# Performance work log

Hardware: AMD Instinct MI355X
Metric: run time of the kernel (lower is better)

Reference implementation:

```python
import jax, jax.numpy as jnp
import numpy as np

B_, L_, D_, N_ = 4, 4096, 1024, 32


def setup_inputs() -> dict:
    key = jax.random.key(0)
    ks = jax.random.split(key, 8)
    def n(k, shape, s=0.02):
        return jax.random.normal(k, shape, jnp.float32) * s
    return {
        "x": jax.random.normal(ks[0], (B_, L_, D_), jnp.float32),
        "in_w": n(ks[1], (2 * D_, D_)),
        "in_b": jnp.zeros((2 * D_,), jnp.float32),
        "conv_w": n(ks[2], (D_, 1, 4), 0.1),
        "conv_b": jnp.zeros((D_,), jnp.float32),
        "A_log": -2.0 + 0.1 * jax.random.normal(ks[3], (D_, N_), jnp.float32),
        "B_w": n(ks[4], (N_, D_)),
        "B_b": jnp.zeros((N_,), jnp.float32),
        "C_w": n(ks[5], (N_, D_)),
        "C_b": jnp.zeros((N_,), jnp.float32),
        "out_w": n(ks[6], (D_, D_)),
        "out_b": jnp.zeros((D_,), jnp.float32),
        "ln_w": jnp.ones((D_,), jnp.float32),
        "ln_b": jnp.zeros((D_,), jnp.float32),
    }


def reference(x, in_w, in_b, conv_w, conv_b, A_log, B_w, B_b, C_w, C_b, out_w, out_b, ln_w, ln_b):
    Bsz, L, D = x.shape
    residual = x
    # in_proj and chunk
    xz = x @ in_w.T + in_b                       # (B, L, 2D)
    xa, z = xz[..., :D], xz[..., D:]
    # depthwise conv1d, kernel=4, padding=2 -> length L+1 (matches torch)
    xc = jax.lax.conv_general_dilated(
        xa.transpose(0, 2, 1), conv_w, (1,), [(2, 2)],
        feature_group_count=D, dimension_numbers=("NCH", "OIH", "NCH"))
    xc = xc + conv_b[None, :, None]
    xc = jax.nn.silu(xc.transpose(0, 2, 1))      # (B, L+1, D)
    A = -jnp.exp(jnp.clip(A_log, -5.0, 2.0))     # (D, N)
    Bm = xc @ B_w.T + B_b                        # (B, L+1, N)
    Cm = xc @ C_w.T + C_b                        # (B, L+1, N)
    # only first L steps are used by the loop
    xs = (xc[:, :L].transpose(1, 0, 2),          # (L, B, D)
          Bm[:, :L].transpose(1, 0, 2),          # (L, B, N)
          Cm[:, :L].transpose(1, 0, 2))          # (L, B, N)
    s0 = jnp.zeros((Bsz, D, A.shape[1]), x.dtype)

    def step(s, t):
        x_t, b_t, c_t = t
        s = jnp.clip(s * A + b_t[:, None, :] * x_t[:, :, None], -10.0, 10.0)
        y = jnp.sum(c_t[:, None, :] * s, axis=-1)  # (B, D)
        return s, y

    _, ys = jax.lax.scan(step, s0, xs)           # ys: (L, B, D)
    y = ys.transpose(1, 0, 2) * jax.nn.silu(z)   # (B, L, D)
    out = y @ out_w.T + out_b
    h = out + residual
    mu = jnp.mean(h, axis=-1, keepdims=True)
    var = jnp.var(h, axis=-1, keepdims=True)
    return (h - mu) / jnp.sqrt(var + 1e-5) * ln_w + ln_b
```

## Files before the change

kernel.cpp:

```cpp
#include <hip/hip_runtime.h>
#include <hip/hip_bf16.h>

#define B_ 4
#define L_ 4096
#define D_ 1024
#define N_ 32
#define MTOT (B_*L_)
#define TCH 32
#define WARM 6
#define STEPS (TCH + WARM)
#define SROWS 48

typedef __bf16 bf16;
typedef __attribute__((ext_vector_type(8))) __bf16 bf16x8;
typedef __attribute__((ext_vector_type(4))) __bf16 bf16x4;
typedef __attribute__((ext_vector_type(4))) float f32x4;
typedef __attribute__((ext_vector_type(2))) float f32x2;

__device__ __forceinline__ void gload_lds16(const void* gsrc, void* ldst) {
  __builtin_amdgcn_global_load_lds(
      (__attribute__((address_space(1))) void*)(unsigned long long)gsrc,
      (__attribute__((address_space(3))) void*)ldst, 16, 0, 0);
}

#define BARR  do { __builtin_amdgcn_s_barrier(); \
                   __builtin_amdgcn_sched_barrier(0); } while (0)
#define LGKM0 do { asm volatile("s_waitcnt lgkmcnt(0)" ::: "memory"); \
                   __builtin_amdgcn_sched_barrier(0); } while (0)

__global__ __launch_bounds__(256) void cvt_w_kernel(
    const float* __restrict__ in_w, const float* __restrict__ out_w,
    const float* __restrict__ B_w, const float* __restrict__ C_w,
    const float* __restrict__ A_log, const float* __restrict__ B_b,
    const float* __restrict__ C_b, const float* __restrict__ x,
    bf16* __restrict__ in_wb, bf16* __restrict__ out_wb, bf16* __restrict__ bcw,
    float* __restrict__ Aexp, float* __restrict__ bias_bc,
    bf16* __restrict__ xb) {
  const int stride = gridDim.x * 256;
  const int i0 = blockIdx.x * 256 + threadIdx.x;
  for (int j = i0; j < (B_ * L_ * D_) / 4; j += stride) {
    const float4 v = ((const float4*)x)[j];
    bf16x4 o = {(bf16)v.x, (bf16)v.y, (bf16)v.z, (bf16)v.w};
    ((bf16x4*)xb)[j] = o;
  }
  for (int j = i0; j < 2 * D_ * D_; j += stride) in_wb[j] = (bf16)in_w[j];
  for (int j = i0; j < D_ * D_; j += stride) out_wb[j] = (bf16)out_w[j];
  for (int j = i0; j < N_ * D_; j += stride) {
    bcw[j] = (bf16)B_w[j];
    bcw[N_ * D_ + j] = (bf16)C_w[j];
  }
  for (int j = i0; j < D_ * N_; j += stride)
    Aexp[j] = -expf(fminf(fmaxf(A_log[j], -5.f), 2.f));
  if (i0 < N_) { bias_bc[i0] = B_b[i0]; bias_bc[N_ + i0] = C_b[i0]; }
}

template <bool OUT_BF16>
__global__ __launch_bounds__(256) void gemm8_kernel(
    const bf16* __restrict__ Ag, const bf16* __restrict__ Wg,
    const float* __restrict__ bias, void* __restrict__ Cg,
    int Ncols, int K, int nbm, int nbn) {
  constexpr int BK = 64;
  __shared__ bf16 As[2][128][64];
  __shared__ bf16 Bs[2][128][64];
  const int tid = threadIdx.x;
  const int lane = tid & 63;
  const int wid = tid >> 6;
  const int wm = wid >> 1, wn = wid & 1;
  const int l15 = lane & 15, lh = lane >> 4, r7 = l15 & 7;

  const int sx = nbm >> 3;
  const int xcd = blockIdx.x & 7;
  const int pos = blockIdx.x >> 3;
  const int bx = xcd * sx + pos / nbn;
  const int by = pos % nbn;
  const int row0 = bx * 128, col0 = by * 128;
  const int nt = K / BK;

  const bf16* aSrc[4]; const bf16* bSrc[4]; int dstOff[4];
#pragma unroll
  for (int j = 0; j < 4; ++j) {
    const int c = tid + j * 256;
    const int row = c >> 3, lcol = c & 7;
    const int gcol = lcol ^ (row & 7);
    aSrc[j] = Ag + (size_t)(row0 + row) * K + gcol * 8;
    bSrc[j] = Wg + (size_t)(col0 + row) * K + gcol * 8;
    dstOff[j] = c * 8;
  }

  f32x4 acc[4][4] = {};

#pragma unroll
  for (int j = 0; j < 4; ++j) gload_lds16(aSrc[j], &As[0][0][0] + dstOff[j]);
#pragma unroll
  for (int j = 0; j < 4; ++j) gload_lds16(bSrc[j], &Bs[0][0][0] + dstOff[j]);
#pragma unroll
  for (int j = 0; j < 4; ++j) gload_lds16(aSrc[j] + BK, &As[1][0][0] + dstOff[j]);
#pragma unroll
  for (int j = 0; j < 4; ++j) gload_lds16(bSrc[j] + BK, &Bs[1][0][0] + dstOff[j]);
  asm volatile("s_waitcnt vmcnt(8)" ::: "memory");
  __builtin_amdgcn_sched_barrier(0);
  BARR;

  for (int t = 0; t < nt; ++t) {
    const int p = t & 1;
    const bf16* Ab = &As[p][0][0];
    const bf16* Bb = &Bs[p][0][0];
    bf16x8 af[4][2], bfr[4][2];
#pragma unroll
    for (int mi = 0; mi < 4; ++mi)
#pragma unroll
      for (int kk = 0; kk < 2; ++kk)
        af[mi][kk] = *(const bf16x8*)(Ab + (wm * 64 + mi * 16 + l15) * 64 +
                                      (((kk * 4 + lh) ^ r7) * 8));
#pragma unroll
    for (int ni = 0; ni < 4; ++ni)
#pragma unroll
      for (int kk = 0; kk < 2; ++kk)
        bfr[ni][kk] = *(const bf16x8*)(Bb + (wn * 64 + ni * 16 + l15) * 64 +
                                       (((kk * 4 + lh) ^ r7) * 8));
    LGKM0;
    BARR;
    if (t + 2 < nt) {
      const int k2 = (t + 2) * BK;
#pragma unroll
      for (int j = 0; j < 4; ++j) gload_lds16(aSrc[j] + k2, &As[p][0][0] + dstOff[j]);
#pragma unroll
      for (int j = 0; j < 4; ++j) gload_lds16(bSrc[j] + k2, &Bs[p][0][0] + dstOff[j]);
    }
    __builtin_amdgcn_s_setprio(1);
#pragma unroll
    for (int kk = 0; kk < 2; ++kk)
#pragma unroll
      for (int mi = 0; mi < 4; ++mi)
#pragma unroll
        for (int ni = 0; ni < 4; ++ni)
          acc[mi][ni] = __builtin_amdgcn_mfma_f32_16x16x32_bf16(
              af[mi][kk], bfr[ni][kk], acc[mi][ni], 0, 0, 0);
    __builtin_amdgcn_s_setprio(0);
    if (t + 2 < nt) asm volatile("s_waitcnt vmcnt(8)" ::: "memory");
    else            asm volatile("s_waitcnt vmcnt(0)" ::: "memory");
    __builtin_amdgcn_sched_barrier(0);
    BARR;
  }

#pragma unroll
  for (int mi = 0; mi < 4; ++mi) {
#pragma unroll
    for (int ni = 0; ni < 4; ++ni) {
      const int c = col0 + wn * 64 + ni * 16 + l15;
      const float bv = bias[c];
#pragma unroll
      for (int j = 0; j < 4; ++j) {
        const int r = row0 + wm * 64 + mi * 16 + lh * 4 + j;
        const float v = acc[mi][ni][j] + bv;
        if constexpr (OUT_BF16) ((bf16*)Cg)[(size_t)r * Ncols + c] = (bf16)v;
        else                    ((float*)Cg)[(size_t)r * Ncols + c] = v;
      }
    }
  }
}

__global__ __launch_bounds__(256) void gemmbc_kernel(
    const bf16* __restrict__ Ag, const bf16* __restrict__ Wg,
    const float* __restrict__ bias, float* __restrict__ Cg, int K) {
  constexpr int BK = 64;
  __shared__ bf16 As[2][64][64];
  __shared__ bf16 Bs[2][64][64];
  const int tid = threadIdx.x;
  const int lane = tid & 63;
  const int wid = tid >> 6;
  const int wm = wid >> 1, wn = wid & 1;
  const int l15 = lane & 15, lh = lane >> 4;
  const int row0 = blockIdx.x * 64;
  const int nt = K / BK;

  const bf16* aSrc[2]; const bf16* bSrc[2]; int dstOff[2];
#pragma unroll
  for (int j = 0; j < 2; ++j) {
    const int c = tid + j * 256;
    const int row = c >> 3, lcol = c & 7;
    const int gcol = lcol ^ (row & 7);
    aSrc[j] = Ag + (size_t)(row0 + row) * K + gcol * 8;
    bSrc[j] = Wg + (size_t)row * K + gcol * 8;
    dstOff[j] = c * 8;
  }

  f32x4 acc[2][2] = {};

#pragma unroll
  for (int j = 0; j < 2; ++j) gload_lds16(aSrc[j], &As[0][0][0] + dstOff[j]);
#pragma unroll
  for (int j = 0; j < 2; ++j) gload_lds16(bSrc[j], &Bs[0][0][0] + dstOff[j]);
#pragma unroll
  for (int j = 0; j < 2; ++j) gload_lds16(aSrc[j] + BK, &As[1][0][0] + dstOff[j]);
#pragma unroll
  for (int j = 0; j < 2; ++j) gload_lds16(bSrc[j] + BK, &Bs[1][0][0] + dstOff[j]);
  asm volatile("s_waitcnt vmcnt(4)" ::: "memory");
  __builtin_amdgcn_sched_barrier(0);
  BARR;

  for (int t = 0; t < nt; ++t) {
    const int p = t & 1;
    const bf16* Ab = &As[p][0][0];
    const bf16* Bb = &Bs[p][0][0];
    bf16x8 af[2][2], bfr[2][2];
#pragma unroll
    for (int mi = 0; mi < 2; ++mi)
#pragma unroll
      for (int kk = 0; kk < 2; ++kk) {
        const int r = wm * 32 + mi * 16 + l15;
        af[mi][kk] = *(const bf16x8*)(Ab + r * 64 + (((kk * 4 + lh) ^ (r & 7)) * 8));
      }
#pragma unroll
    for (int ni = 0; ni < 2; ++ni)
#pragma unroll
      for (int kk = 0; kk < 2; ++kk) {
        const int r = wn * 32 + ni * 16 + l15;
        bfr[ni][kk] = *(const bf16x8*)(Bb + r * 64 + (((kk * 4 + lh) ^ (r & 7)) * 8));
      }
    LGKM0;
    BARR;
    if (t + 2 < nt) {
      const int k2 = (t + 2) * BK;
#pragma unroll
      for (int j = 0; j < 2; ++j) gload_lds16(aSrc[j] + k2, &As[p][0][0] + dstOff[j]);
#pragma unroll
      for (int j = 0; j < 2; ++j) gload_lds16(bSrc[j] + k2, &Bs[p][0][0] + dstOff[j]);
    }
    __builtin_amdgcn_s_setprio(1);
#pragma unroll
    for (int kk = 0; kk < 2; ++kk)
#pragma unroll
      for (int mi = 0; mi < 2; ++mi)
#pragma unroll
        for (int ni = 0; ni < 2; ++ni)
          acc[mi][ni] = __builtin_amdgcn_mfma_f32_16x16x32_bf16(
              af[mi][kk], bfr[ni][kk], acc[mi][ni], 0, 0, 0);
    __builtin_amdgcn_s_setprio(0);
    if (t + 2 < nt) asm volatile("s_waitcnt vmcnt(4)" ::: "memory");
    else            asm volatile("s_waitcnt vmcnt(0)" ::: "memory");
    __builtin_amdgcn_sched_barrier(0);
    BARR;
  }

#pragma unroll
  for (int mi = 0; mi < 2; ++mi) {
#pragma unroll
    for (int ni = 0; ni < 2; ++ni) {
      const int c = wn * 32 + ni * 16 + l15;
      const float bv = bias[c];
#pragma unroll
      for (int j = 0; j < 4; ++j) {
        const int r = row0 + wm * 32 + mi * 16 + lh * 4 + j;
        Cg[(size_t)r * 64 + c] = acc[mi][ni][j] + bv;
      }
    }
  }
}

__global__ __launch_bounds__(512, 1) void gemm256_kernel(
    const bf16* __restrict__ Ag, const bf16* __restrict__ Wg,
    const float* __restrict__ bias, bf16* __restrict__ Cg,
    int Ncols, int K, int nbm, int nbn) {
  __shared__ bf16 lds[8][128][64];
  const int tid = threadIdx.x;
  const int lane = tid & 63;
  const int wid = tid >> 6;
  const int wm = wid >> 2;
  const int wn = wid & 3;
  const int l15 = lane & 15, lh = lane >> 4;

  const int sx = nbm >> 3;
  const int xcd = blockIdx.x & 7;
  const int pos = blockIdx.x >> 3;
  const int bx = xcd * sx + pos / nbn;
  const int by = pos % nbn;
  const int row0 = bx * 256, col0 = by * 256;
  const int nt = K / 64;

  const bf16* aS0; const bf16* aS1; const bf16* bS0; const bf16* bS1;
  int dO0, dO1;
  {
    const int c0 = tid, c1 = tid + 512;
    const int r0 = c0 >> 3, r1 = c1 >> 3;
    const int g0 = (c0 & 7) ^ (r0 & 7), g1 = (c1 & 7) ^ (r1 & 7);
    aS0 = Ag + (size_t)(row0 + r0) * K + g0 * 8;
    aS1 = Ag + (size_t)(row0 + r1) * K + g1 * 8;
    bS0 = Wg + (size_t)(col0 + r0) * K + g0 * 8;
    bS1 = Wg + (size_t)(col0 + r1) * K + g1 * 8;
    dO0 = c0 * 8; dO1 = c1 * 8;
  }

#define STAGE_A(T, HALF) do {                                               \
    const size_t off_ = (size_t)(HALF) * 128 * K + (size_t)(T) * 64;        \
    bf16* dst_ = &lds[((T) & 1) * 4 + (HALF)][0][0];                        \
    gload_lds16(aS0 + off_, dst_ + dO0);                                    \
    gload_lds16(aS1 + off_, dst_ + dO1); } while (0)
#define STAGE_B(T, HALF) do {                                               \
    const size_t off_ = (size_t)(HALF) * 128 * K + (size_t)(T) * 64;        \
    bf16* dst_ = &lds[((T) & 1) * 4 + 2 + (HALF)][0][0];                    \
    gload_lds16(bS0 + off_, dst_ + dO0);                                    \
    gload_lds16(bS1 + off_, dst_ + dO1); } while (0)

  f32x4 acc[8][4] = {};

  STAGE_A(0, 0); STAGE_A(0, 1); STAGE_B(0, 0); STAGE_B(0, 1);
  STAGE_B(1, 0); STAGE_B(1, 1);
  asm volatile("s_waitcnt vmcnt(4)" ::: "memory");
  __builtin_amdgcn_sched_barrier(0);
  BARR;

  for (int T = 0; T < nt; ++T) {
    const int p = T & 1;
    const bf16* Aseg = &lds[p * 4 + wm][0][0];
    const bf16* Bseg = &lds[p * 4 + 2 + (wn >> 1)][0][0];
    const int brow0 = (wn & 1) * 64;
    bf16x8 af[4][2], bfv[4][2];
    const bool s1 = (T + 1 < nt), s2 = (T + 2 < nt);

    if (s1) STAGE_A(T + 1, 0);
#pragma unroll
    for (int mi = 0; mi < 4; ++mi) {
      const int r = mi * 16 + l15, sw = r & 7;
      af[mi][0] = *(const bf16x8*)(Aseg + r * 64 + ((lh ^ sw)) * 8);
      af[mi][1] = *(const bf16x8*)(Aseg + r * 64 + (((4 + lh) ^ sw)) * 8);
    }
#pragma unroll
    for (int ni = 0; ni < 2; ++ni) {
      const int r = brow0 + ni * 16 + l15, sw = r & 7;
      bfv[ni][0] = *(const bf16x8*)(Bseg + r * 64 + ((lh ^ sw)) * 8);
      bfv[ni][1] = *(const bf16x8*)(Bseg + r * 64 + (((4 + lh) ^ sw)) * 8);
    }
    BARR; LGKM0;
    __builtin_amdgcn_s_setprio(1);
#pragma unroll
    for (int kk = 0; kk < 2; ++kk)
#pragma unroll
      for (int mi = 0; mi < 4; ++mi)
#pragma unroll
        for (int ni = 0; ni < 2; ++ni)
          acc[mi][ni] = __builtin_amdgcn_mfma_f32_16x16x32_bf16(
              af[mi][kk], bfv[ni][kk], acc[mi][ni], 0, 0, 0);
    __builtin_amdgcn_s_setprio(0);
    BARR;

    if (s1) STAGE_A(T + 1, 1);
#pragma unroll
    for (int ni = 2; ni < 4; ++ni) {
      const int r = brow0 + ni * 16 + l15, sw = r & 7;
      bfv[ni][0] = *(const bf16x8*)(Bseg + r * 64 + ((lh ^ sw)) * 8);
      bfv[ni][1] = *(const bf16x8*)(Bseg + r * 64 + (((4 + lh) ^ sw)) * 8);
    }
    BARR; LGKM0;
    __builtin_amdgcn_s_setprio(1);
#pragma unroll
    for (int kk = 0; kk < 2; ++kk)
#pragma unroll
      for (int mi = 0; mi < 4; ++mi)
#pragma unroll
        for (int ni = 2; ni < 4; ++ni)
          acc[mi][ni] = __builtin_amdgcn_mfma_f32_16x16x32_bf16(
              af[mi][kk], bfv[ni][kk], acc[mi][ni], 0, 0, 0);
    __builtin_amdgcn_s_setprio(0);
    BARR;

    if (s2) STAGE_B(T + 2, 0);
#pragma unroll
    for (int mi = 0; mi < 4; ++mi) {
      const int r = (mi + 4) * 16 + l15, sw = r & 7;
      af[mi][0] = *(const bf16x8*)(Aseg + r * 64 + ((lh ^ sw)) * 8);
      af[mi][1] = *(const bf16x8*)(Aseg + r * 64 + (((4 + lh) ^ sw)) * 8);
    }
    BARR; LGKM0;
    __builtin_amdgcn_s_setprio(1);
#pragma unroll
    for (int kk = 0; kk < 2; ++kk)
#pragma unroll
      for (int mi = 0; mi < 4; ++mi)
#pragma unroll
        for (int ni = 0; ni < 2; ++ni)
          acc[mi + 4][ni] = __builtin_amdgcn_mfma_f32_16x16x32_bf16(
              af[mi][kk], bfv[ni][kk], acc[mi + 4][ni], 0, 0, 0);
    __builtin_amdgcn_s_setprio(0);
    BARR;

    if (s2) STAGE_B(T + 2, 1);
    BARR;
    __builtin_amdgcn_s_setprio(1);
#pragma unroll
    for (int kk = 0; kk < 2; ++kk)
#pragma unroll
      for (int mi = 0; mi < 4; ++mi)
#pragma unroll
        for (int ni = 2; ni < 4; ++ni)
          acc[mi + 4][ni] = __builtin_amdgcn_mfma_f32_16x16x32_bf16(
              af[mi][kk], bfv[ni][kk], acc[mi + 4][ni], 0, 0, 0);
    __builtin_amdgcn_s_setprio(0);
    if (s2) asm volatile("s_waitcnt vmcnt(4)" ::: "memory");
    else    asm volatile("s_waitcnt vmcnt(0)" ::: "memory");
    __builtin_amdgcn_sched_barrier(0);
    BARR;
  }
#undef STAGE_A
#undef STAGE_B

#pragma unroll
  for (int mi = 0; mi < 8; ++mi) {
#pragma unroll
    for (int ni = 0; ni < 4; ++ni) {
      const int c = col0 + wn * 64 + ni * 16 + l15;
      const float bv = bias[c];
#pragma unroll
      for (int j = 0; j < 4; ++j) {
        const int r = row0 + wm * 128 + mi * 16 + lh * 4 + j;
        Cg[(size_t)r * Ncols + c] = (bf16)(acc[mi][ni][j] + bv);
      }
    }
  }
}

__global__ __launch_bounds__(256) void conv_silu_kernel(
    const bf16* __restrict__ xz, const float* __restrict__ conv_w,
    const float* __restrict__ conv_b, bf16* __restrict__ xc) {
  const int idx = blockIdx.x * 256 + threadIdx.x;
  const int d8 = idx & (D_ / 8 - 1);
  const int bt = idx >> 7;
  const int t = bt & (L_ - 1);
  const int b = bt >> 12;
  const int d = d8 * 8;

  float accv[8];
  float4 w4[8];
#pragma unroll
  for (int j = 0; j < 8; ++j) {
    accv[j] = conv_b[d + j];
    w4[j] = *(const float4*)(conv_w + (size_t)(d + j) * 4);
  }
#pragma unroll
  for (int k = 0; k < 4; ++k) {
    const int tt = t + k - 2;
    if (tt < 0 || tt >= L_) continue;
    const bf16x8 xv = *(const bf16x8*)(xz + (size_t)(b * L_ + tt) * (2 * D_) + d);
#pragma unroll
    for (int j = 0; j < 8; ++j) {
      const float wk = (k == 0) ? w4[j].x : (k == 1) ? w4[j].y : (k == 2) ? w4[j].z : w4[j].w;
      accv[j] += (float)xv[j] * wk;
    }
  }
  bf16x8 o;
#pragma unroll
  for (int j = 0; j < 8; ++j) {
    const float v = accv[j];
    o[j] = (bf16)(v / (1.f + __expf(-v)));
  }
  *(bf16x8*)(xc + (size_t)(b * L_ + t) * D_ + d) = o;
}

#define SCAN_STEP(PB, PC, XT)                                             \
  {                                                                       \
    const f32x2 xt2 = {XT, XT};                                           \
    yac = (f32x2){0.f, 0.f};                                              \
    _Pragma("unroll")                                                     \
    for (int q = 0; q < 8; ++q) {                                         \
      f32x2 v = __builtin_elementwise_fma(s[q], Ar[q], PB[q] * xt2);      \
      s[q] = v;                                                           \
      yac = __builtin_elementwise_fma(PC[q], v, yac);                     \
    }                                                                     \
  }

__device__ __forceinline__ void load8v(f32x2* dst, const float* p) {
#pragma unroll
  for (int q = 0; q < 4; ++q) {
    const f32x4 v = ((const f32x4*)p)[q];
    dst[2 * q]     = (f32x2){v.x, v.y};
    dst[2 * q + 1] = (f32x2){v.z, v.w};
  }
}

__global__ __launch_bounds__(256)
__attribute__((amdgpu_waves_per_eu(4)))
void scan_kernel(
    const bf16* __restrict__ xc, const float* __restrict__ BC,
    const bf16* __restrict__ xz, const float* __restrict__ Aexp,
    bf16* __restrict__ y) {
  const int dg = blockIdx.x, chunk = blockIdx.y, b = blockIdx.z;
  const int tid = threadIdx.x;
  const int wid = tid >> 6;
  const int nh = tid & 1;
  const int dl = tid >> 1;
  const int d = dg * 128 + dl;
  const int t0 = chunk * TCH;
  const int warm = (t0 >= WARM) ? WARM : 0;
  const int tstart = t0 - warm;

  __shared__ float bcs[SROWS][64];
  __shared__ bf16 xcs[SROWS][128];
  __shared__ bf16 zs[TCH][128];

#pragma unroll
  for (int i = 0; i < 3; ++i)
    gload_lds16(BC + ((size_t)b * L_ + tstart) * 64 + (size_t)(tid + i * 256) * 4,
                (float*)&bcs[0][0] + (size_t)(wid * 64 + i * 256) * 4);
#pragma unroll
  for (int i = 0; i < 3; ++i) {
    const int c = tid + i * 256;
    gload_lds16(xc + ((size_t)b * L_ + tstart + (c >> 4)) * D_ + dg * 128 + (c & 15) * 8,
                (bf16*)&xcs[0][0] + (size_t)(wid * 64 + i * 256) * 8);
  }
#pragma unroll
  for (int i = 0; i < 2; ++i) {
    const int c = tid + i * 256;
    gload_lds16(xz + ((size_t)b * L_ + t0 + (c >> 4)) * (2 * D_) + D_ + dg * 128 + (c & 15) * 8,
                (bf16*)&zs[0][0] + (size_t)(wid * 64 + i * 256) * 8);
  }

  f32x2 Ar[8], s[8];
  {
    const f32x2* ap = (const f32x2*)(Aexp + (size_t)d * N_ + nh * 16);
#pragma unroll
    for (int q = 0; q < 8; ++q) { Ar[q] = ap[q]; s[q] = (f32x2){0.f, 0.f}; }
  }

  bf16* yp = y + (size_t)b * L_ * D_ + d;
  f32x2 yac;

  __syncthreads();

  for (int i = 0; i < warm; ++i) {
    const float xt = (float)xcs[i][dl];
    const f32x2 xt2 = {xt, xt};
    const f32x2* rb = (const f32x2*)&bcs[i][nh * 16];
#pragma unroll
    for (int q = 0; q < 8; ++q)
      s[q] = __builtin_elementwise_fma(s[q], Ar[q], rb[q] * xt2);
  }

  f32x2 pbA[8], pcA[8], pbB[8], pcB[8];
  float pxA, pzA, pxB, pzB;
  load8v(pbA, &bcs[warm][nh * 16]);
  load8v(pcA, &bcs[warm][32 + nh * 16]);
  pxA = (float)xcs[warm][dl];
  pzA = (float)zs[0][dl];

  for (int j = 0; j < TCH; j += 2) {
    load8v(pbB, &bcs[warm + j + 1][nh * 16]);
    load8v(pcB, &bcs[warm + j + 1][32 + nh * 16]);
    pxB = (float)xcs[warm + j + 1][dl];
    pzB = (float)zs[j + 1][dl];
    SCAN_STEP(pbA, pcA, pxA);
    {
      float yacc = yac.x + yac.y;
      yacc += __shfl_xor(yacc, 1);
      if (nh == 0) {
        const float sz = pzA / (1.f + __expf(-pzA));
        yp[(size_t)(t0 + j) * D_] = (bf16)(yacc * sz);
      }
    }
    load8v(pbA, &bcs[warm + j + 2][nh * 16]);
    load8v(pcA, &bcs[warm + j + 2][32 + nh * 16]);
    pxA = (float)xcs[warm + j + 2][dl];
    pzA = (float)zs[(j + 2 < TCH) ? (j + 2) : 0][dl];
    SCAN_STEP(pbB, pcB, pxB);
    {
      float yacc = yac.x + yac.y;
      yacc += __shfl_xor(yacc, 1);
      if (nh == 0) {
        const float sz = pzB / (1.f + __expf(-pzB));
        yp[(size_t)(t0 + j + 1) * D_] = (bf16)(yacc * sz);
      }
    }
  }
}

__global__ __launch_bounds__(256) void ln2_kernel(const bf16* __restrict__ g,
                                                  const float* __restrict__ x,
                                                  const float* __restrict__ ln_w,
                                                  const float* __restrict__ ln_b,
                                                  float* __restrict__ out) {
  const int row = blockIdx.x;
  const int tid = threadIdx.x;
  const bf16x4 gv = ((const bf16x4*)(g + (size_t)row * D_))[tid];
  const float4 xv = ((const float4*)(x + (size_t)row * D_))[tid];
  float4 v;
  v.x = (float)gv[0] + xv.x;
  v.y = (float)gv[1] + xv.y;
  v.z = (float)gv[2] + xv.z;
  v.w = (float)gv[3] + xv.w;
  float sum = v.x + v.y + v.z + v.w;
  float sq = v.x * v.x + v.y * v.y + v.z * v.z + v.w * v.w;
#pragma unroll
  for (int off = 32; off >= 1; off >>= 1) {
    sum += __shfl_xor(sum, off);
    sq += __shfl_xor(sq, off);
  }
  __shared__ float red[8];
  const int wid = tid >> 6;
  if ((tid & 63) == 0) { red[wid] = sum; red[4 + wid] = sq; }
  __syncthreads();
  sum = red[0] + red[1] + red[2] + red[3];
  sq = red[4] + red[5] + red[6] + red[7];
  const float mu = sum * (1.f / D_);
  const float var = sq * (1.f / D_) - mu * mu;
  const float inv = rsqrtf(var + 1e-5f);
  const float4 w4 = ((const float4*)ln_w)[tid];
  const float4 b4 = ((const float4*)ln_b)[tid];
  float4 o;
  o.x = (v.x - mu) * inv * w4.x + b4.x;
  o.y = (v.y - mu) * inv * w4.y + b4.y;
  o.z = (v.z - mu) * inv * w4.z + b4.z;
  o.w = (v.w - mu) * inv * w4.w + b4.w;
  ((float4*)(out + (size_t)row * D_))[tid] = o;
}

extern "C" void kernel_launch(void* const* d_in, const int* in_sizes, int n_in,
                              void* d_out, int out_size, void* d_ws, size_t ws_size,
                              hipStream_t stream) {
  (void)in_sizes; (void)n_in; (void)out_size; (void)ws_size;
  const float* x      = (const float*)d_in[0];
  const float* in_w   = (const float*)d_in[1];
  const float* in_b   = (const float*)d_in[2];
  const float* conv_w = (const float*)d_in[3];
  const float* conv_b = (const float*)d_in[4];
  const float* A_log  = (const float*)d_in[5];
  const float* B_w    = (const float*)d_in[6];
  const float* B_b    = (const float*)d_in[7];
  const float* C_w    = (const float*)d_in[8];
  const float* C_b    = (const float*)d_in[9];
  const float* out_w  = (const float*)d_in[10];
  const float* out_b  = (const float*)d_in[11];
  const float* ln_w   = (const float*)d_in[12];
  const float* ln_b   = (const float*)d_in[13];
  float* out = (float*)d_out;

  char* ws = (char*)d_ws;
  bf16* xb_y    = (bf16*)(ws + 0);
  bf16* xz      = (bf16*)(ws + 33554432);
  bf16* xc_g    = (bf16*)(ws + 100663296);
  float* BC     = (float*)(ws + 134217728);
  bf16* in_wb   = (bf16*)(ws + 138412032);
  bf16* out_wb  = (bf16*)(ws + 142606336);
  bf16* bcw     = (bf16*)(ws + 144703488);
  float* Aexp   = (float*)(ws + 144834560);
  float* bias_bc= (float*)(ws + 144965632);

  cvt_w_kernel<<<2048, 256, 0, stream>>>(in_w, out_w, B_w, C_w, A_log, B_b, C_b,
                                         x, in_wb, out_wb, bcw, Aexp, bias_bc, xb_y);
  gemm8_kernel<true>
      <<<128 * 16, 256, 0, stream>>>(xb_y, in_wb, in_b, xz, 2 * D_, D_, 128, 16);
  conv_silu_kernel<<<(B_ * L_ * D_ / 8) / 256, 256, 0, stream>>>(xz, conv_w, conv_b, xc_g);
  gemmbc_kernel<<<MTOT / 64, 256, 0, stream>>>(xc_g, bcw, bias_bc, BC, D_);
  scan_kernel<<<dim3(D_ / 128, L_ / TCH, B_), 256, 0, stream>>>(xc_g, BC, xz, Aexp, xb_y);
  gemm256_kernel<<<64 * 4, 512, 0, stream>>>(xb_y, out_wb, out_b, xc_g,
                                             D_, D_, 64, 4);
  ln2_kernel<<<MTOT, 256, 0, stream>>>(xc_g, x, ln_w, ln_b, out);
}
```

Baseline: 294.4 us.

## Write scan output into xz's x-half, keep bf16 x for residual in LayerNorm

The scan now writes y into the unused first half of the xz buffer, with a row stride of 2D, and the output GEMM reads A through a new lda parameter. The original bf16 copy of x is therefore kept intact, and the final LayerNorm reads that bf16 residual instead of the fp32 input, halving the residual read traffic. The scan kernel's waves_per_eu hint is loosened to a 2–4 range. The risks are lower residual precision from using bf16 instead of fp32, and a strided A access pattern in the GEMM.

```diff
diff --git a/kernel.cpp b/kernel.cpp
--- a/kernel.cpp
+++ b/kernel.cpp
@@ -261,7 +261,7 @@
 __global__ __launch_bounds__(512, 1) void gemm256_kernel(
     const bf16* __restrict__ Ag, const bf16* __restrict__ Wg,
     const float* __restrict__ bias, bf16* __restrict__ Cg,
-    int Ncols, int K, int nbm, int nbn) {
+    int Ncols, int K, int lda, int nbm, int nbn) {
   __shared__ bf16 lds[8][128][64];
   const int tid = threadIdx.x;
   const int lane = tid & 63;
@@ -284,15 +284,15 @@
     const int c0 = tid, c1 = tid + 512;
     const int r0 = c0 >> 3, r1 = c1 >> 3;
     const int g0 = (c0 & 7) ^ (r0 & 7), g1 = (c1 & 7) ^ (r1 & 7);
-    aS0 = Ag + (size_t)(row0 + r0) * K + g0 * 8;
-    aS1 = Ag + (size_t)(row0 + r1) * K + g1 * 8;
+    aS0 = Ag + (size_t)(row0 + r0) * lda + g0 * 8;
+    aS1 = Ag + (size_t)(row0 + r1) * lda + g1 * 8;
     bS0 = Wg + (size_t)(col0 + r0) * K + g0 * 8;
     bS1 = Wg + (size_t)(col0 + r1) * K + g1 * 8;
     dO0 = c0 * 8; dO1 = c1 * 8;
   }
 
 #define STAGE_A(T, HALF) do {                                               \
-    const size_t off_ = (size_t)(HALF) * 128 * K + (size_t)(T) * 64;        \
+    const size_t off_ = (size_t)(HALF) * 128 * lda + (size_t)(T) * 64;      \
     bf16* dst_ = &lds[((T) & 1) * 4 + (HALF)][0][0];                        \
     gload_lds16(aS0 + off_, dst_ + dO0);                                    \
     gload_lds16(aS1 + off_, dst_ + dO1); } while (0)
@@ -478,11 +478,11 @@
 }
 
 __global__ __launch_bounds__(256)
-__attribute__((amdgpu_waves_per_eu(4)))
+__attribute__((amdgpu_waves_per_eu(2, 4)))
 void scan_kernel(
     const bf16* __restrict__ xc, const float* __restrict__ BC,
     const bf16* __restrict__ xz, const float* __restrict__ Aexp,
-    bf16* __restrict__ y) {
+    bf16* __restrict__ yz) {
   const int dg = blockIdx.x, chunk = blockIdx.y, b = blockIdx.z;
   const int tid = threadIdx.x;
   const int wid = tid >> 6;
@@ -521,7 +521,7 @@
     for (int q = 0; q < 8; ++q) { Ar[q] = ap[q]; s[q] = (f32x2){0.f, 0.f}; }
   }
 
-  bf16* yp = y + (size_t)b * L_ * D_ + d;
+  bf16* yp = yz + (size_t)b * L_ * (2 * D_) + d;
   f32x2 yac;
 
   __syncthreads();
@@ -553,7 +553,7 @@
       yacc += __shfl_xor(yacc, 1);
       if (nh == 0) {
         const float sz = pzA / (1.f + __expf(-pzA));
-        yp[(size_t)(t0 + j) * D_] = (bf16)(yacc * sz);
+        yp[(size_t)(t0 + j) * (2 * D_)] = (bf16)(yacc * sz);
       }
     }
     load8v(pbA, &bcs[warm + j + 2][nh * 16]);
@@ -566,26 +566,26 @@
       yacc += __shfl_xor(yacc, 1);
       if (nh == 0) {
         const float sz = pzB / (1.f + __expf(-pzB));
-        yp[(size_t)(t0 + j + 1) * D_] = (bf16)(yacc * sz);
+        yp[(size_t)(t0 + j + 1) * (2 * D_)] = (bf16)(yacc * sz);
       }
     }
   }
 }
 
 __global__ __launch_bounds__(256) void ln2_kernel(const bf16* __restrict__ g,
-                                                  const float* __restrict__ x,
+                                                  const bf16* __restrict__ xb,
                                                   const float* __restrict__ ln_w,
                                                   const float* __restrict__ ln_b,
                                                   float* __restrict__ out) {
   const int row = blockIdx.x;
   const int tid = threadIdx.x;
   const bf16x4 gv = ((const bf16x4*)(g + (size_t)row * D_))[tid];
-  const float4 xv = ((const float4*)(x + (size_t)row * D_))[tid];
+  const bf16x4 xv = ((const bf16x4*)(xb + (size_t)row * D_))[tid];
   float4 v;
-  v.x = (float)gv[0] + xv.x;
-  v.y = (float)gv[1] + xv.y;
-  v.z = (float)gv[2] + xv.z;
-  v.w = (float)gv[3] + xv.w;
+  v.x = (float)gv[0] + (float)xv[0];
+  v.y = (float)gv[1] + (float)xv[1];
+  v.z = (float)gv[2] + (float)xv[2];
+  v.w = (float)gv[3] + (float)xv[3];
   float sum = v.x + v.y + v.z + v.w;
   float sq = v.x * v.x + v.y * v.y + v.z * v.z + v.w * v.w;
 #pragma unroll
@@ -633,7 +633,7 @@
   float* out = (float*)d_out;
 
   char* ws = (char*)d_ws;
-  bf16* xb_y    = (bf16*)(ws + 0);
+  bf16* xb      = (bf16*)(ws + 0);
   bf16* xz      = (bf16*)(ws + 33554432);
   bf16* xc_g    = (bf16*)(ws + 100663296);
   float* BC     = (float*)(ws + 134217728);
@@ -644,13 +644,13 @@
   float* bias_bc= (float*)(ws + 144965632);
 
   cvt_w_kernel<<<2048, 256, 0, stream>>>(in_w, out_w, B_w, C_w, A_log, B_b, C_b,
-                                         x, in_wb, out_wb, bcw, Aexp, bias_bc, xb_y);
+                                         x, in_wb, out_wb, bcw, Aexp, bias_bc, xb);
   gemm8_kernel<true>
-      <<<128 * 16, 256, 0, stream>>>(xb_y, in_wb, in_b, xz, 2 * D_, D_, 128, 16);
+      <<<128 * 16, 256, 0, stream>>>(xb, in_wb, in_b, xz, 2 * D_, D_, 128, 16);
   conv_silu_kernel<<<(B_ * L_ * D_ / 8) / 256, 256, 0, stream>>>(xz, conv_w, conv_b, xc_g);
   gemmbc_kernel<<<MTOT / 64, 256, 0, stream>>>(xc_g, bcw, bias_bc, BC, D_);
-  scan_kernel<<<dim3(D_ / 128, L_ / TCH, B_), 256, 0, stream>>>(xc_g, BC, xz, Aexp, xb_y);
-  gemm256_kernel<<<64 * 4, 512, 0, stream>>>(xb_y, out_wb, out_b, xc_g,
-                                             D_, D_, 64, 4);
-  ln2_kernel<<<MTOT, 256, 0, stream>>>(xc_g, x, ln_w, ln_b, out);
-}
+  scan_kernel<<<dim3(D_ / 128, L_ / TCH, B_), 256, 0, stream>>>(xc_g, BC, xz, Aexp, xz);
+  gemm256_kernel<<<64 * 4, 512, 0, stream>>>(xz, out_wb, out_b, xc_g,
+                                             D_, D_, 2 * D_, 64, 4);
+  ln2_kernel<<<MTOT, 256, 0, stream>>>(xc_g, xb, ln_w, ln_b, out);
+}
```

New measurement: 290.9 us. Within noise of the previous version (-1.2%).
